# Performance work log

Hardware: AMD Instinct MI355X
Metric: run time of the kernel (lower is better)

The kernel has to match this reference:

```python
import jax, jax.numpy as jnp
import numpy as np

DOF = 7
DT = 0.1
MAX_VEL = 20.0
ACTION_RANGE = 50.0
BATCH = 16384


def skew(w):
    x, y, z = w[..., 0], w[..., 1], w[..., 2]
    o = jnp.zeros_like(x)
    return jnp.stack([jnp.stack([o, -z, y], -1),
                      jnp.stack([z, o, -x], -1),
                      jnp.stack([-y, x, o], -1)], -2)


def exp6(xi):
    # xi: (..., 6) twist [omega, v] (angular first). General se(3) exponential.
    w, v = xi[..., :3], xi[..., 3:]
    th = jnp.linalg.norm(w, axis=-1)                     # (...)
    small = th < 1e-10
    th_s = jnp.where(small, 1.0, th)
    W = skew(w / th_s[..., None])
    W2 = W @ W
    s, c = jnp.sin(th), jnp.cos(th)
    I3 = jnp.eye(3, dtype=xi.dtype)
    R = I3 + s[..., None, None] * W + (1.0 - c)[..., None, None] * W2
    Gm = th[..., None, None] * I3 + (1.0 - c)[..., None, None] * W + (th - s)[..., None, None] * W2
    p = jnp.einsum('...ij,...j->...i', Gm, v / th_s[..., None])
    R = jnp.where(small[..., None, None], I3, R)
    p = jnp.where(small[..., None], v, p)
    top = jnp.concatenate([R, p[..., None]], -1)
    bot = jnp.broadcast_to(jnp.array([0., 0., 0., 1.], xi.dtype), top.shape[:-2] + (1, 4))
    return jnp.concatenate([top, bot], -2)


def trans_inv(T):
    R = T[..., :3, :3]
    p = T[..., :3, 3]
    Rt = jnp.swapaxes(R, -1, -2)
    pi = -jnp.einsum('...ij,...j->...i', Rt, p)
    top = jnp.concatenate([Rt, pi[..., None]], -1)
    bot = jnp.broadcast_to(jnp.array([0., 0., 0., 1.], T.dtype), top.shape[:-2] + (1, 4))
    return jnp.concatenate([top, bot], -2)


def adjoint(T):
    R = T[..., :3, :3]
    p = T[..., :3, 3]
    pR = skew(p) @ R
    z = jnp.zeros_like(R)
    return jnp.concatenate([jnp.concatenate([R, z], -1),
                            jnp.concatenate([pR, R], -1)], -2)


def ad(V):
    w, v = V[..., :3], V[..., 3:]
    W, Vm = skew(w), skew(v)
    z = jnp.zeros_like(W)
    return jnp.concatenate([jnp.concatenate([W, z], -1),
                            jnp.concatenate([Vm, W], -1)], -2)


def inverse_dynamics(q, dq, ddq, gravity, ftip, Mlist, Glist, A):
    # Newton-Euler inverse dynamics (Modern Robotics), batched over B.
    B, n = q.shape
    dt = q.dtype
    V = jnp.zeros((B, 6), dt)
    Vd = jnp.concatenate([jnp.zeros((B, 3), dt), -jnp.broadcast_to(gravity, (B, 3))], -1)
    AdTs, Vs, Vds = [], [], []
    for i in range(n):  # forward recursion over joints (small fixed dof)
        Ti = exp6(-A[i] * q[:, i, None]) @ trans_inv(Mlist[i])   # (B,4,4)
        AdTi = adjoint(Ti)                                       # (B,6,6)
        V = jnp.einsum('bij,bj->bi', AdTi, V) + A[i] * dq[:, i, None]
        Vd = (jnp.einsum('bij,bj->bi', AdTi, Vd) + A[i] * ddq[:, i, None]
              + jnp.einsum('bij,j->bi', ad(V), A[i]) * dq[:, i, None])
        AdTs.append(AdTi)
        Vs.append(V)
        Vds.append(Vd)
    AdTs.append(jnp.broadcast_to(adjoint(trans_inv(Mlist[n])), (B, 6, 6)))
    F = jnp.broadcast_to(ftip, (B, 6))
    taus = [None] * n
    for i in range(n - 1, -1, -1):  # backward recursion
        GV = jnp.einsum('ij,bj->bi', Glist[i], Vs[i])
        F = (jnp.einsum('bji,bj->bi', AdTs[i + 1], F)
             + jnp.einsum('ij,bj->bi', Glist[i], Vds[i])
             - jnp.einsum('bji,bj->bi', ad(Vs[i]), GV))
        taus[i] = jnp.sum(F * A[i], -1)
    return jnp.stack(taus, -1)  # (B, n)


def forward_dynamics(q, dq, tau, gravity, ftip, Mlist, Glist, A):
    n = q.shape[1]
    z = jnp.zeros_like(q)
    g0 = jnp.zeros(3, q.dtype)
    f0 = jnp.zeros(6, q.dtype)
    # mass matrix columns via unit-ddq inverse dynamics
    cols = jax.vmap(lambda e: inverse_dynamics(q, z, jnp.broadcast_to(e, q.shape),
                                               g0, f0, Mlist, Glist, A))(jnp.eye(n, dtype=q.dtype))
    Mmat = jnp.transpose(cols, (1, 2, 0))                        # (B,n,n)
    # coriolis + gravity + end-effector bias in one pass (ddq=0)
    h = inverse_dynamics(q, dq, z, gravity, ftip, Mlist, Glist, A)
    return jnp.linalg.solve(Mmat, (tau - h)[..., None])[..., 0]


def _forward(state, torque, M_param, A, G_param, gravity, ftip):
    n = DOF
    # M property: keep top 3 rows, force bottom row to [0,0,0,1]
    bot = jnp.broadcast_to(jnp.array([0., 0., 0., 1.], M_param.dtype), (n + 1, 1, 4))
    Mlist = jnp.concatenate([M_param[:, :3], bot], axis=1)       # (n+1,4,4)
    # G property: diag(Ixx,Iyy,Izz,m,m,m)
    dvec = jnp.concatenate([G_param[:, :3], jnp.repeat(G_param[:, 3:4], 3, axis=1)], -1)
    Glist = dvec[:, :, None] * jnp.eye(6, dtype=G_param.dtype)   # (n,6,6)
    tau = torque * ACTION_RANGE

    def derivs(s, t):
        qpos, qvel, qf = s[..., :n], s[..., n:2 * n], s[..., 2 * n:3 * n]
        qacc = forward_dynamics(qpos, qvel, qf, gravity, ftip, Mlist, Glist, A)
        return jnp.concatenate([qvel, qacc, jnp.zeros_like(qf)], -1)

    s0 = jnp.concatenate([state, tau], -1)
    dt = DT
    k1 = derivs(s0, 0.0)
    k2 = derivs(s0 + 0.5 * dt * k1, 0.5 * dt)
    k3 = derivs(s0 + 0.5 * dt * k2, 0.5 * dt)
    k4 = derivs(s0 + dt * k3, dt)
    s1 = s0 + (dt / 6.0) * (k1 + 2.0 * k2 + 2.0 * k3 + k4)
    ns = s1[..., :2 * n]
    q = (ns[..., :n] + jnp.pi) % (2.0 * jnp.pi) - jnp.pi
    dq = jnp.clip(ns[..., n:], -MAX_VEL, MAX_VEL)
    # fk_in_space: chain link transforms, last frame is end-effector
    B = q.shape[0]
    T = jnp.broadcast_to(jnp.eye(4, dtype=q.dtype), (B, 4, 4))
    for i in range(n):
        T = T @ Mlist[i] @ exp6(A[i] * q[:, i, None])
    T = T @ Mlist[n]
    ee = T[:, :3, 3]
    return jnp.concatenate([q, dq], -1), ee


def setup_inputs() -> dict:
    key = jax.random.key(0)
    ks = jax.random.split(key, 6)
    state = jax.random.normal(ks[0], (BATCH, 2 * DOF), jnp.float32)
    torque = jax.random.normal(ks[1], (BATCH, DOF), jnp.float32)
    M_param = jnp.eye(4, dtype=jnp.float32)[None] + 0.05 * jax.random.normal(ks[2], (DOF + 1, 4, 4), jnp.float32)
    A = jax.random.uniform(ks[3], (DOF, 6), jnp.float32)
    G_param = jax.random.uniform(ks[4], (DOF, 4), jnp.float32, minval=0.1, maxval=1.0)
    gravity = jnp.array([0.0, -9.8, 0.0], jnp.float32)
    ftip = jnp.zeros(6, jnp.float32)
    return {"state": state, "torque": torque, "M_param": M_param, "A": A,
            "G_param": G_param, "gravity": gravity, "ftip": ftip}


def reference(state, torque, M_param, A, G_param, gravity, ftip):
    return _forward(state, torque, M_param, A, G_param, gravity, ftip)
```

## Files before the change

### kernel.cpp

```cpp
#include <hip/hip_runtime.h>
#include <math.h>

#define NB 16384

struct SConsts {
  float MrT[8][9];
  float mp[8][3];
  float A[7][6];
  float Gd[7][6];
  float X7p[3];
  float g[3];
  float ftip[6];
};

__device__ __forceinline__ void syncw() {
  __builtin_amdgcn_sched_barrier(0);
  __builtin_amdgcn_wave_barrier();
  __builtin_amdgcn_sched_barrier(0);
}

__device__ __forceinline__ float dot6(const float* a, const float* b) {
  return a[0]*b[0]+a[1]*b[1]+a[2]*b[2]+a[3]*b[3]+a[4]*b[4]+a[5]*b[5];
}

__device__ __forceinline__ void exp6_dev(float wx, float wy, float wz,
                                         float vx, float vy, float vz,
                                         float R[9], float p[3]) {
  float th2 = wx*wx + wy*wy + wz*wz;
  float th  = __builtin_amdgcn_sqrtf(th2);
  bool sm = th < 1e-10f;
  float ths = sm ? 1.0f : th;
  float inv = __builtin_amdgcn_rcpf(ths);
  float ux = wx*inv, uy = wy*inv, uz = wz*inv;
  float s = __sinf(th);
  float c = __cosf(th);
  float omc = 1.0f - c;
  float r00 = c + omc*ux*ux;
  float r01 = omc*ux*uy - s*uz;
  float r02 = omc*ux*uz + s*uy;
  float r10 = omc*uy*ux + s*uz;
  float r11 = c + omc*uy*uy;
  float r12 = omc*uy*uz - s*ux;
  float r20 = omc*uz*ux - s*uy;
  float r21 = omc*uz*uy + s*ux;
  float r22 = c + omc*uz*uz;
  float k1 = omc*inv, k2 = (th - s)*inv;
  float cx = uy*vz - uz*vy, cy = uz*vx - ux*vz, cz = ux*vy - uy*vx;
  float udv = ux*vx + uy*vy + uz*vz;
  float px = vx + k1*cx + k2*(ux*udv - vx);
  float py = vy + k1*cy + k2*(uy*udv - vy);
  float pz = vz + k1*cz + k2*(uz*udv - vz);
  R[0]=sm?1.f:r00; R[1]=sm?0.f:r01; R[2]=sm?0.f:r02;
  R[3]=sm?0.f:r10; R[4]=sm?1.f:r11; R[5]=sm?0.f:r12;
  R[6]=sm?0.f:r20; R[7]=sm?0.f:r21; R[8]=sm?1.f:r22;
  p[0]=sm?vx:px; p[1]=sm?vy:py; p[2]=sm?vz:pz;
}

__device__ __forceinline__ void Xapply(const float* R, const float* p,
                                       const float in[6], float out[6]) {
  float a = R[0]*in[0]+R[1]*in[1]+R[2]*in[2];
  float b = R[3]*in[0]+R[4]*in[1]+R[5]*in[2];
  float c = R[6]*in[0]+R[7]*in[1]+R[8]*in[2];
  float d = R[0]*in[3]+R[1]*in[4]+R[2]*in[5];
  float e = R[3]*in[3]+R[4]*in[4]+R[5]*in[5];
  float f = R[6]*in[3]+R[7]*in[4]+R[8]*in[5];
  out[0]=a; out[1]=b; out[2]=c;
  out[3] = p[1]*c - p[2]*b + d;
  out[4] = p[2]*a - p[0]*c + e;
  out[5] = p[0]*b - p[1]*a + f;
}

__device__ __forceinline__ void XTapply(const float* R, const float* p,
                                        const float in[6], float out[6]) {
  float fx=in[3], fy=in[4], fz=in[5];
  float tx = in[0] - (p[1]*fz - p[2]*fy);
  float ty = in[1] - (p[2]*fx - p[0]*fz);
  float tz = in[2] - (p[0]*fy - p[1]*fx);
  out[0] = R[0]*tx + R[3]*ty + R[6]*tz;
  out[1] = R[1]*tx + R[4]*ty + R[7]*tz;
  out[2] = R[2]*tx + R[5]*ty + R[8]*tz;
  out[3] = R[0]*fx + R[3]*fy + R[6]*fz;
  out[4] = R[1]*fx + R[4]*fy + R[7]*fz;
  out[5] = R[2]*fx + R[5]*fy + R[8]*fz;
}

extern "C" __global__ void __launch_bounds__(64, 2)
arm_kernel(const float* __restrict__ state, const float* __restrict__ torque,
           const float* __restrict__ Mp, const float* __restrict__ Ain,
           const float* __restrict__ Gp, const float* __restrict__ grav,
           const float* __restrict__ ftip_in, float* __restrict__ out)
{
  __shared__ SConsts C;
  __shared__ float XL[8][100];
  __shared__ float CL[8][68];
  const int t = threadIdx.x;

  {
    int i = t >> 3;
    #pragma unroll
    for (int kk = (t & 7); kk < 12; kk += 8) {
      if (kk < 9) {
        int r = kk / 3, c = kk - 3*(kk/3);
        C.MrT[i][c*3 + r] = Mp[i*16 + r*4 + c];
      } else {
        int r = kk - 9;
        C.mp[i][r] = Mp[i*16 + r*4 + 3];
      }
    }
    if (t < 42) {
      int i2 = t / 6, k = t - 6*(t/6);
      C.A[i2][k] = Ain[t];
      C.Gd[i2][k] = (k < 3) ? Gp[i2*4 + k] : Gp[i2*4 + 3];
    }
    if (t < 3) C.g[t] = grav[t];
    if (t < 6) C.ftip[t] = ftip_in[t];
  }
  syncw();
  if (t < 3)
    C.X7p[t] = -(C.MrT[7][t*3+0]*C.mp[7][0] + C.MrT[7][t*3+1]*C.mp[7][1] + C.MrT[7][t*3+2]*C.mp[7][2]);
  syncw();

  const int sub = t & 7;
  const int e   = t >> 3;
  const int b   = blockIdx.x * 8 + e;
  const int subc = (sub < 7) ? sub : 6;

  float dq0[7], tau[7], dqs[7];
  #pragma unroll
  for (int k = 0; k < 7; ++k) {
    dq0[k] = state[b*14 + 7 + k];
    tau[k] = torque[b*7 + k] * 50.0f;
    dqs[k] = dq0[k];
  }
  float q0s  = state[b*14 + subc];
  float dq0s = dq0[0];
  #pragma unroll
  for (int k = 1; k < 7; ++k) dq0s = (subc == k) ? dq0[k] : dq0s;

  float qss = q0s, dqss = dq0s;
  float accqs = 0.0f, accdqs = 0.0f;
  float a[7];
  const float gm = (sub == 7) ? 1.0f : 0.0f;

  #pragma unroll 1
  for (int stage = 0; stage < 4; ++stage) {
    syncw();
    if (sub < 7) {
      float Re[9], pe[3];
      exp6_dev(-C.A[sub][0]*qss, -C.A[sub][1]*qss, -C.A[sub][2]*qss,
               -C.A[sub][3]*qss, -C.A[sub][4]*qss, -C.A[sub][5]*qss, Re, pe);
      float Xr[12];
      #pragma unroll
      for (int r = 0; r < 3; ++r) {
        #pragma unroll
        for (int c = 0; c < 3; ++c)
          Xr[r*3+c] = Re[r*3+0]*C.MrT[sub][0+c] + Re[r*3+1]*C.MrT[sub][3+c] + Re[r*3+2]*C.MrT[sub][6+c];
      }
      #pragma unroll
      for (int r = 0; r < 3; ++r)
        Xr[9+r] = pe[r] - (Xr[r*3+0]*C.mp[sub][0] + Xr[r*3+1]*C.mp[sub][1] + Xr[r*3+2]*C.mp[sub][2]);
      float4* dst = (float4*)&XL[e][sub*12];
      dst[0] = make_float4(Xr[0],Xr[1],Xr[2],Xr[3]);
      dst[1] = make_float4(Xr[4],Xr[5],Xr[6],Xr[7]);
      dst[2] = make_float4(Xr[8],Xr[9],Xr[10],Xr[11]);
    }
    syncw();

    float X[7][12];
    #pragma unroll
    for (int i = 0; i < 7; ++i) {
      const float4* sx = (const float4*)&XL[e][i*12];
      float4 x0 = sx[0], x1 = sx[1], x2 = sx[2];
      X[i][0]=x0.x; X[i][1]=x0.y; X[i][2]=x0.z; X[i][3]=x0.w;
      X[i][4]=x1.x; X[i][5]=x1.y; X[i][6]=x1.z; X[i][7]=x1.w;
      X[i][8]=x2.x; X[i][9]=x2.y; X[i][10]=x2.z; X[i][11]=x2.w;
    }

    float V[6] = {0,0,0,0,0,0};
    float Vd[6];
    Vd[0]=0.0f; Vd[1]=0.0f; Vd[2]=0.0f;
    Vd[3] = -gm*C.g[0]; Vd[4] = -gm*C.g[1]; Vd[5] = -gm*C.g[2];
    float Fb[7][6];
    #pragma unroll
    for (int i = 0; i < 7; ++i) {
      float dqi  = (sub == 7) ? dqs[i] : 0.0f;
      float ddqi = (sub == i) ? 1.0f : 0.0f;
      float tv[6];
      Xapply(X[i], X[i]+9, V, tv);
      #pragma unroll
      for (int k = 0; k < 6; ++k) V[k] = tv[k] + C.A[i][k]*dqi;
      Xapply(X[i], X[i]+9, Vd, tv);
      float wx=V[0],wy=V[1],wz=V[2],vx=V[3],vy=V[4],vz=V[5];
      float ax=C.A[i][0],ay=C.A[i][1],az=C.A[i][2];
      float bx=C.A[i][3],by=C.A[i][4],bz=C.A[i][5];
      Vd[0] = tv[0] + ax*ddqi + (wy*az - wz*ay)*dqi;
      Vd[1] = tv[1] + ay*ddqi + (wz*ax - wx*az)*dqi;
      Vd[2] = tv[2] + az*ddqi + (wx*ay - wy*ax)*dqi;
      Vd[3] = tv[3] + bx*ddqi + (vy*az - vz*ay + wy*bz - wz*by)*dqi;
      Vd[4] = tv[4] + by*ddqi + (vz*ax - vx*az + wz*bx - wx*bz)*dqi;
      Vd[5] = tv[5] + bz*ddqi + (vx*ay - vy*ax + wx*by - wy*bx)*dqi;
      float g0=C.Gd[i][0], g1=C.Gd[i][1], g2=C.Gd[i][2], m=C.Gd[i][3];
      float Gt0=g0*wx, Gt1=g1*wy, Gt2=g2*wz;
      float Gb0=m*vx,  Gb1=m*vy,  Gb2=m*vz;
      Fb[i][0] = g0*Vd[0] + (wy*Gt2 - wz*Gt1) + (vy*Gb2 - vz*Gb1);
      Fb[i][1] = g1*Vd[1] + (wz*Gt0 - wx*Gt2) + (vz*Gb0 - vx*Gb2);
      Fb[i][2] = g2*Vd[2] + (wx*Gt1 - wy*Gt0) + (vx*Gb1 - vy*Gb0);
      Fb[i][3] = m*Vd[3] + (wy*Gb2 - wz*Gb1);
      Fb[i][4] = m*Vd[4] + (wz*Gb0 - wx*Gb2);
      Fb[i][5] = m*Vd[5] + (wx*Gb1 - wy*Gb0);
    }
    float col[7];
    float F[6];
    #pragma unroll
    for (int k = 0; k < 6; ++k) F[k] = gm*C.ftip[k];
    #pragma unroll
    for (int i = 6; i >= 0; --i) {
      float tv[6];
      if (i == 6) XTapply(C.MrT[7], C.X7p, F, tv);
      else        XTapply(X[i+1], X[i+1]+9, F, tv);
      #pragma unroll
      for (int k = 0; k < 6; ++k) F[k] = tv[k] + Fb[i][k];
      col[i] = dot6(F, C.A[i]);
    }

    syncw();
    #pragma unroll
    for (int k = 0; k < 7; ++k) CL[e][k*8 + sub] = col[k];
    syncw();
    float Mm[7][7], rhs[7];
    #pragma unroll
    for (int i = 0; i < 7; ++i) {
      const float4* rp = (const float4*)&CL[e][i*8];
      float4 r0 = rp[0], r1 = rp[1];
      Mm[i][0]=r0.x; Mm[i][1]=r0.y; Mm[i][2]=r0.z; Mm[i][3]=r0.w;
      Mm[i][4]=r1.x; Mm[i][5]=r1.y; Mm[i][6]=r1.z;
      rhs[i] = tau[i] - r1.w;
    }

    float invd[7];
    #pragma unroll
    for (int k = 0; k < 7; ++k) {
      invd[k] = __builtin_amdgcn_rcpf(Mm[k][k]);
      #pragma unroll
      for (int i2 = k+1; i2 < 7; ++i2) {
        float f = Mm[i2][k] * invd[k];
        #pragma unroll
        for (int c2 = k+1; c2 < 7; ++c2) Mm[i2][c2] -= f * Mm[k][c2];
        rhs[i2] -= f * rhs[k];
      }
    }
    #pragma unroll
    for (int i2 = 6; i2 >= 0; --i2) {
      float s = rhs[i2];
      #pragma unroll
      for (int c2 = i2+1; c2 < 7; ++c2) s -= Mm[i2][c2] * a[c2];
      a[i2] = s * invd[i2];
    }

    float a_own = a[0];
    #pragma unroll
    for (int k = 1; k < 7; ++k) a_own = (subc == k) ? a[k] : a_own;
    float w = (stage == 1 || stage == 2) ? 2.0f : 1.0f;
    accqs  += w*dqss;
    accdqs += w*a_own;
    if (stage < 3) {
      float cc = (stage == 2) ? 0.1f : 0.05f;
      qss  = q0s + cc*dqss;
      dqss = dq0s + cc*a_own;
      #pragma unroll
      for (int k = 0; k < 7; ++k) dqs[k] = dq0[k] + cc*a[k];
    }
  }

  const float c6 = (float)(0.1/6.0);
  const float PI_F = 3.14159265358979323846f;
  const float TWO_PI_F = 6.28318530717958647692f;
  const float INV_TWO_PI_F = 0.15915494309189535f;
  float q1 = q0s  + c6*accqs;
  float d1 = dq0s + c6*accdqs;
  float x = q1 + PI_F;
  float n = floorf(x * INV_TWO_PI_F);
  float y = fmaf(n, -TWO_PI_F, x);
  y = (y < 0.0f) ? y + TWO_PI_F : y;
  y = (y >= TWO_PI_F) ? y - TWO_PI_F : y;
  float qw_own  = y - PI_F;
  float dqw_own = fminf(fmaxf(d1, -20.0f), 20.0f);
  if (sub < 7) {
    out[b*14 + sub]     = qw_own;
    out[b*14 + 7 + sub] = dqw_own;
  }

  syncw();
  if (sub < 7) {
    float Re[9], pe[3];
    exp6_dev(C.A[sub][0]*qw_own, C.A[sub][1]*qw_own, C.A[sub][2]*qw_own,
             C.A[sub][3]*qw_own, C.A[sub][4]*qw_own, C.A[sub][5]*qw_own, Re, pe);
    float L[12];
    #pragma unroll
    for (int r = 0; r < 3; ++r) {
      #pragma unroll
      for (int c = 0; c < 3; ++c)
        L[r*3+c] = C.MrT[sub][0*3+r]*Re[0*3+c] + C.MrT[sub][1*3+r]*Re[1*3+c] + C.MrT[sub][2*3+r]*Re[2*3+c];
      L[9+r] = C.MrT[sub][0*3+r]*pe[0] + C.MrT[sub][1*3+r]*pe[1] + C.MrT[sub][2*3+r]*pe[2] + C.mp[sub][r];
    }
    float4* dst = (float4*)&XL[e][sub*12];
    dst[0] = make_float4(L[0],L[1],L[2],L[3]);
    dst[1] = make_float4(L[4],L[5],L[6],L[7]);
    dst[2] = make_float4(L[8],L[9],L[10],L[11]);
  }
  syncw();
  float X2[7][12];
  #pragma unroll
  for (int i = 0; i < 7; ++i) {
    const float4* sx = (const float4*)&XL[e][i*12];
    float4 x0 = sx[0], x1 = sx[1], x2 = sx[2];
    X2[i][0]=x0.x; X2[i][1]=x0.y; X2[i][2]=x0.z; X2[i][3]=x0.w;
    X2[i][4]=x1.x; X2[i][5]=x1.y; X2[i][6]=x1.z; X2[i][7]=x1.w;
    X2[i][8]=x2.x; X2[i][9]=x2.y; X2[i][10]=x2.z; X2[i][11]=x2.w;
  }
  float v0 = C.mp[7][0], v1 = C.mp[7][1], v2 = C.mp[7][2];
  #pragma unroll
  for (int i = 6; i >= 0; --i) {
    float n0 = X2[i][0]*v0 + X2[i][1]*v1 + X2[i][2]*v2 + X2[i][9];
    float n1 = X2[i][3]*v0 + X2[i][4]*v1 + X2[i][5]*v2 + X2[i][10];
    float n2 = X2[i][6]*v0 + X2[i][7]*v1 + X2[i][8]*v2 + X2[i][11];
    v0 = n0; v1 = n1; v2 = n2;
  }
  {
    float ev = v0;
    ev = (sub == 1) ? v1 : ev;
    ev = (sub == 2) ? v2 : ev;
    if (sub < 3) out[NB*14 + b*3 + sub] = ev;
  }
}

extern "C" void kernel_launch(void* const* d_in, const int* in_sizes, int n_in,
                              void* d_out, int out_size, void* d_ws, size_t ws_size,
                              hipStream_t stream) {
  const float* state  = (const float*)d_in[0];
  const float* torque = (const float*)d_in[1];
  const float* Mp     = (const float*)d_in[2];
  const float* Ain    = (const float*)d_in[3];
  const float* Gp     = (const float*)d_in[4];
  const float* grav   = (const float*)d_in[5];
  const float* ftip   = (const float*)d_in[6];
  float* out = (float*)d_out;
  hipLaunchKernelGGL(arm_kernel, dim3(NB/8), dim3(64), 0, stream,
                     state, torque, Mp, Ain, Gp, grav, ftip, out);
}
```

Before: 26.53 us.

## Replace backward force recursion with shared-memory Jacobian-based mass matrix columns

The backward Newton-Euler force pass is replaced. Each sub-lane stores its per-link unit-acceleration twist in shared memory, and mass-matrix columns are then formed as dot products of the link wrenches with the stored twists, plus a tip-force term. The 7x12 transform arrays are no longer kept in registers; rows are re-read from LDS where needed, which lowers register pressure. The cost is a large shared-memory buffer of about 12.5 KB per block and many LDS reads, which may limit occupancy or bank bandwidth.

```diff
diff --git a/kernel.cpp b/kernel.cpp
--- a/kernel.cpp
+++ b/kernel.cpp
@@ -70,20 +70,6 @@
   out[5] = p[0]*b - p[1]*a + f;
 }
 
-__device__ __forceinline__ void XTapply(const float* R, const float* p,
-                                        const float in[6], float out[6]) {
-  float fx=in[3], fy=in[4], fz=in[5];
-  float tx = in[0] - (p[1]*fz - p[2]*fy);
-  float ty = in[1] - (p[2]*fx - p[0]*fz);
-  float tz = in[2] - (p[0]*fy - p[1]*fx);
-  out[0] = R[0]*tx + R[3]*ty + R[6]*tz;
-  out[1] = R[1]*tx + R[4]*ty + R[7]*tz;
-  out[2] = R[2]*tx + R[5]*ty + R[8]*tz;
-  out[3] = R[0]*fx + R[3]*fy + R[6]*fz;
-  out[4] = R[1]*fx + R[4]*fy + R[7]*fz;
-  out[5] = R[2]*fx + R[5]*fy + R[8]*fz;
-}
-
 extern "C" __global__ void __launch_bounds__(64, 2)
 arm_kernel(const float* __restrict__ state, const float* __restrict__ torque,
            const float* __restrict__ Mp, const float* __restrict__ Ain,
@@ -93,6 +79,8 @@
   __shared__ SConsts C;
   __shared__ float XL[8][100];
   __shared__ float CL[8][68];
+  __shared__ float JL[8*7*7*8];
+  __shared__ float TD[8][8];
   const int t = threadIdx.x;
 
   {
@@ -166,16 +154,6 @@
     }
     syncw();
 
-    float X[7][12];
-    #pragma unroll
-    for (int i = 0; i < 7; ++i) {
-      const float4* sx = (const float4*)&XL[e][i*12];
-      float4 x0 = sx[0], x1 = sx[1], x2 = sx[2];
-      X[i][0]=x0.x; X[i][1]=x0.y; X[i][2]=x0.z; X[i][3]=x0.w;
-      X[i][4]=x1.x; X[i][5]=x1.y; X[i][6]=x1.z; X[i][7]=x1.w;
-      X[i][8]=x2.x; X[i][9]=x2.y; X[i][10]=x2.z; X[i][11]=x2.w;
-    }
-
     float V[6] = {0,0,0,0,0,0};
     float Vd[6];
     Vd[0]=0.0f; Vd[1]=0.0f; Vd[2]=0.0f;
@@ -183,13 +161,16 @@
     float Fb[7][6];
     #pragma unroll
     for (int i = 0; i < 7; ++i) {
+      const float4* sx = (const float4*)&XL[e][i*12];
+      float4 x0 = sx[0], x1 = sx[1], x2 = sx[2];
+      float Xr[12] = {x0.x,x0.y,x0.z,x0.w, x1.x,x1.y,x1.z,x1.w, x2.x,x2.y,x2.z,x2.w};
       float dqi  = (sub == 7) ? dqs[i] : 0.0f;
       float ddqi = (sub == i) ? 1.0f : 0.0f;
       float tv[6];
-      Xapply(X[i], X[i]+9, V, tv);
+      Xapply(Xr, Xr+9, V, tv);
       #pragma unroll
       for (int k = 0; k < 6; ++k) V[k] = tv[k] + C.A[i][k]*dqi;
-      Xapply(X[i], X[i]+9, Vd, tv);
+      Xapply(Xr, Xr+9, Vd, tv);
       float wx=V[0],wy=V[1],wz=V[2],vx=V[3],vy=V[4],vz=V[5];
       float ax=C.A[i][0],ay=C.A[i][1],az=C.A[i][2];
       float bx=C.A[i][3],by=C.A[i][4],bz=C.A[i][5];
@@ -199,6 +180,11 @@
       Vd[3] = tv[3] + bx*ddqi + (vy*az - vz*ay + wy*bz - wz*by)*dqi;
       Vd[4] = tv[4] + by*ddqi + (vz*ax - vx*az + wz*bx - wx*bz)*dqi;
       Vd[5] = tv[5] + bz*ddqi + (vx*ay - vy*ax + wx*by - wy*bx)*dqi;
+      if (sub < 7) {
+        float* jp = &JL[((e*7 + i)*7 + sub)*8];
+        *(float4*)jp = make_float4(Vd[0], Vd[1], Vd[2], Vd[3]);
+        *(float2*)(jp + 4) = make_float2(Vd[4], Vd[5]);
+      }
       float g0=C.Gd[i][0], g1=C.Gd[i][1], g2=C.Gd[i][2], m=C.Gd[i][3];
       float Gt0=g0*wx, Gt1=g1*wy, Gt2=g2*wz;
       float Gb0=m*vx,  Gb1=m*vy,  Gb2=m*vz;
@@ -209,21 +195,29 @@
       Fb[i][4] = m*Vd[4] + (wz*Gb0 - wx*Gb2);
       Fb[i][5] = m*Vd[5] + (wx*Gb1 - wy*Gb0);
     }
-    float col[7];
-    float F[6];
-    #pragma unroll
-    for (int k = 0; k < 6; ++k) F[k] = gm*C.ftip[k];
-    #pragma unroll
-    for (int i = 6; i >= 0; --i) {
-      float tv[6];
-      if (i == 6) XTapply(C.MrT[7], C.X7p, F, tv);
-      else        XTapply(X[i+1], X[i+1]+9, F, tv);
-      #pragma unroll
-      for (int k = 0; k < 6; ++k) F[k] = tv[k] + Fb[i][k];
-      col[i] = dot6(F, C.A[i]);
-    }
-
+    {
+      float jt[6];
+      Xapply(C.MrT[7], C.X7p, Vd, jt);
+      float td = dot6(jt, C.ftip);
+      if (sub < 7) TD[e][sub] = td;
+    }
     syncw();
+
+    float col[7] = {0,0,0,0,0,0,0};
+    #pragma unroll
+    for (int k = 0; k < 7; ++k) {
+      #pragma unroll
+      for (int i = 0; i <= k; ++i) {
+        const float* jp = &JL[((e*7 + k)*7 + i)*8];
+        float4 j0 = *(const float4*)jp;
+        float2 j1 = *(const float2*)(jp + 4);
+        col[i] += Fb[k][0]*j0.x + Fb[k][1]*j0.y + Fb[k][2]*j0.z
+                + Fb[k][3]*j0.w + Fb[k][4]*j1.x + Fb[k][5]*j1.y;
+      }
+    }
+    #pragma unroll
+    for (int i = 0; i < 7; ++i) col[i] += gm * TD[e][i];
+
     #pragma unroll
     for (int k = 0; k < 7; ++k) CL[e][k*8 + sub] = col[k];
     syncw();
@@ -309,21 +303,14 @@
     dst[2] = make_float4(L[8],L[9],L[10],L[11]);
   }
   syncw();
-  float X2[7][12];
-  #pragma unroll
-  for (int i = 0; i < 7; ++i) {
-    const float4* sx = (const float4*)&XL[e][i*12];
-    float4 x0 = sx[0], x1 = sx[1], x2 = sx[2];
-    X2[i][0]=x0.x; X2[i][1]=x0.y; X2[i][2]=x0.z; X2[i][3]=x0.w;
-    X2[i][4]=x1.x; X2[i][5]=x1.y; X2[i][6]=x1.z; X2[i][7]=x1.w;
-    X2[i][8]=x2.x; X2[i][9]=x2.y; X2[i][10]=x2.z; X2[i][11]=x2.w;
-  }
   float v0 = C.mp[7][0], v1 = C.mp[7][1], v2 = C.mp[7][2];
   #pragma unroll
   for (int i = 6; i >= 0; --i) {
-    float n0 = X2[i][0]*v0 + X2[i][1]*v1 + X2[i][2]*v2 + X2[i][9];
-    float n1 = X2[i][3]*v0 + X2[i][4]*v1 + X2[i][5]*v2 + X2[i][10];
-    float n2 = X2[i][6]*v0 + X2[i][7]*v1 + X2[i][8]*v2 + X2[i][11];
+    const float4* sx = (const float4*)&XL[e][i*12];
+    float4 x0 = sx[0], x1 = sx[1], x2 = sx[2];
+    float n0 = x0.x*v0 + x0.y*v1 + x0.z*v2 + x2.y;
+    float n1 = x0.w*v0 + x1.x*v1 + x1.y*v2 + x2.z;
+    float n2 = x1.z*v0 + x1.w*v1 + x2.x*v2 + x2.w;
     v0 = n0; v1 = n1; v2 = n2;
   }
   {
```

New measurement: 34.64 us. 30.6% more time.

## Process two batch elements per 8-lane group to raise per-thread ILP

Applied to the files above, without the earlier changes.

Each 8-lane group now handles two batch elements, interleaving their exp6 builds, RNEA passes, 7x7 solves and FK chains. The grid is halved to 1024 blocks and shared buffers are doubled. RNEA now reads the transforms from LDS per step instead of caching them all in registers, and the launch bound drops to one wave minimum. The aim is more independent work per thread to hide latency and to amortise the per-block constant load, at the cost of higher register pressure and fewer waves per CU.

```diff
diff --git a/kernel.cpp b/kernel.cpp
--- a/kernel.cpp
+++ b/kernel.cpp
@@ -84,15 +84,117 @@
   out[5] = R[2]*fx + R[5]*fy + R[8]*fz;
 }
 
-extern "C" __global__ void __launch_bounds__(64, 2)
+__device__ __forceinline__ void build_X(const SConsts& C, int sub, float q,
+                                        float* XLe) {
+  float Re[9], pe[3];
+  exp6_dev(-C.A[sub][0]*q, -C.A[sub][1]*q, -C.A[sub][2]*q,
+           -C.A[sub][3]*q, -C.A[sub][4]*q, -C.A[sub][5]*q, Re, pe);
+  float Xr[12];
+  #pragma unroll
+  for (int r = 0; r < 3; ++r) {
+    #pragma unroll
+    for (int c = 0; c < 3; ++c)
+      Xr[r*3+c] = Re[r*3+0]*C.MrT[sub][0+c] + Re[r*3+1]*C.MrT[sub][3+c] + Re[r*3+2]*C.MrT[sub][6+c];
+  }
+  #pragma unroll
+  for (int r = 0; r < 3; ++r)
+    Xr[9+r] = pe[r] - (Xr[r*3+0]*C.mp[sub][0] + Xr[r*3+1]*C.mp[sub][1] + Xr[r*3+2]*C.mp[sub][2]);
+  float4* dst = (float4*)XLe;
+  dst[0] = make_float4(Xr[0],Xr[1],Xr[2],Xr[3]);
+  dst[1] = make_float4(Xr[4],Xr[5],Xr[6],Xr[7]);
+  dst[2] = make_float4(Xr[8],Xr[9],Xr[10],Xr[11]);
+}
+
+__device__ __forceinline__ void rnea_pass(const SConsts& C, const float* XLe,
+                                          const float dqs[7], int sub, float gm,
+                                          float col[7]) {
+  float V[6] = {0,0,0,0,0,0};
+  float Vd[6];
+  Vd[0]=0.0f; Vd[1]=0.0f; Vd[2]=0.0f;
+  Vd[3] = -gm*C.g[0]; Vd[4] = -gm*C.g[1]; Vd[5] = -gm*C.g[2];
+  float Fb[7][6];
+  #pragma unroll
+  for (int i = 0; i < 7; ++i) {
+    const float4* sx = (const float4*)&XLe[i*12];
+    float4 x0 = sx[0], x1 = sx[1], x2 = sx[2];
+    float Xr[12] = {x0.x,x0.y,x0.z,x0.w, x1.x,x1.y,x1.z,x1.w, x2.x,x2.y,x2.z,x2.w};
+    float dqi  = (sub == 7) ? dqs[i] : 0.0f;
+    float ddqi = (sub == i) ? 1.0f : 0.0f;
+    float tv[6];
+    Xapply(Xr, Xr+9, V, tv);
+    #pragma unroll
+    for (int k = 0; k < 6; ++k) V[k] = tv[k] + C.A[i][k]*dqi;
+    Xapply(Xr, Xr+9, Vd, tv);
+    float wx=V[0],wy=V[1],wz=V[2],vx=V[3],vy=V[4],vz=V[5];
+    float ax=C.A[i][0],ay=C.A[i][1],az=C.A[i][2];
+    float bx=C.A[i][3],by=C.A[i][4],bz=C.A[i][5];
+    Vd[0] = tv[0] + ax*ddqi + (wy*az - wz*ay)*dqi;
+    Vd[1] = tv[1] + ay*ddqi + (wz*ax - wx*az)*dqi;
+    Vd[2] = tv[2] + az*ddqi + (wx*ay - wy*ax)*dqi;
+    Vd[3] = tv[3] + bx*ddqi + (vy*az - vz*ay + wy*bz - wz*by)*dqi;
+    Vd[4] = tv[4] + by*ddqi + (vz*ax - vx*az + wz*bx - wx*bz)*dqi;
+    Vd[5] = tv[5] + bz*ddqi + (vx*ay - vy*ax + wx*by - wy*bx)*dqi;
+    float g0=C.Gd[i][0], g1=C.Gd[i][1], g2=C.Gd[i][2], m=C.Gd[i][3];
+    float Gt0=g0*wx, Gt1=g1*wy, Gt2=g2*wz;
+    float Gb0=m*vx,  Gb1=m*vy,  Gb2=m*vz;
+    Fb[i][0] = g0*Vd[0] + (wy*Gt2 - wz*Gt1) + (vy*Gb2 - vz*Gb1);
+    Fb[i][1] = g1*Vd[1] + (wz*Gt0 - wx*Gt2) + (vz*Gb0 - vx*Gb2);
+    Fb[i][2] = g2*Vd[2] + (wx*Gt1 - wy*Gt0) + (vx*Gb1 - vy*Gb0);
+    Fb[i][3] = m*Vd[3] + (wy*Gb2 - wz*Gb1);
+    Fb[i][4] = m*Vd[4] + (wz*Gb0 - wx*Gb2);
+    Fb[i][5] = m*Vd[5] + (wx*Gb1 - wy*Gb0);
+  }
+  float F[6];
+  #pragma unroll
+  for (int k = 0; k < 6; ++k) F[k] = gm*C.ftip[k];
+  #pragma unroll
+  for (int i = 6; i >= 0; --i) {
+    float tv[6];
+    if (i == 6) {
+      XTapply(C.MrT[7], C.X7p, F, tv);
+    } else {
+      const float4* sx = (const float4*)&XLe[(i+1)*12];
+      float4 x0 = sx[0], x1 = sx[1], x2 = sx[2];
+      float Xr[12] = {x0.x,x0.y,x0.z,x0.w, x1.x,x1.y,x1.z,x1.w, x2.x,x2.y,x2.z,x2.w};
+      XTapply(Xr, Xr+9, F, tv);
+    }
+    #pragma unroll
+    for (int k = 0; k < 6; ++k) F[k] = tv[k] + Fb[i][k];
+    col[i] = dot6(F, C.A[i]);
+  }
+}
+
+__device__ __forceinline__ void solve7(float Mm[7][7], float rhs[7], float a[7]) {
+  float invd[7];
+  #pragma unroll
+  for (int k = 0; k < 7; ++k) {
+    invd[k] = __builtin_amdgcn_rcpf(Mm[k][k]);
+    #pragma unroll
+    for (int i2 = k+1; i2 < 7; ++i2) {
+      float f = Mm[i2][k] * invd[k];
+      #pragma unroll
+      for (int c2 = k+1; c2 < 7; ++c2) Mm[i2][c2] -= f * Mm[k][c2];
+      rhs[i2] -= f * rhs[k];
+    }
+  }
+  #pragma unroll
+  for (int i2 = 6; i2 >= 0; --i2) {
+    float s = rhs[i2];
+    #pragma unroll
+    for (int c2 = i2+1; c2 < 7; ++c2) s -= Mm[i2][c2] * a[c2];
+    a[i2] = s * invd[i2];
+  }
+}
+
+extern "C" __global__ void __launch_bounds__(64, 1)
 arm_kernel(const float* __restrict__ state, const float* __restrict__ torque,
            const float* __restrict__ Mp, const float* __restrict__ Ain,
            const float* __restrict__ Gp, const float* __restrict__ grav,
            const float* __restrict__ ftip_in, float* __restrict__ out)
 {
   __shared__ SConsts C;
-  __shared__ float XL[8][100];
-  __shared__ float CL[8][68];
+  __shared__ float XL[16][100];
+  __shared__ float CL[16][68];
   const int t = threadIdx.x;
 
   {
@@ -118,219 +220,181 @@
   syncw();
   if (t < 3)
     C.X7p[t] = -(C.MrT[7][t*3+0]*C.mp[7][0] + C.MrT[7][t*3+1]*C.mp[7][1] + C.MrT[7][t*3+2]*C.mp[7][2]);
-  syncw();
 
   const int sub = t & 7;
-  const int e   = t >> 3;
-  const int b   = blockIdx.x * 8 + e;
+  const int g   = t >> 3;
+  const int eA  = g*2, eB = g*2 + 1;
+  const int bA  = blockIdx.x * 16 + eA;
+  const int bB  = bA + 1;
   const int subc = (sub < 7) ? sub : 6;
 
-  float dq0[7], tau[7], dqs[7];
+  float dq0A[7], tauA[7], dqsA[7], dq0B[7], tauB[7], dqsB[7];
   #pragma unroll
   for (int k = 0; k < 7; ++k) {
-    dq0[k] = state[b*14 + 7 + k];
-    tau[k] = torque[b*7 + k] * 50.0f;
-    dqs[k] = dq0[k];
-  }
-  float q0s  = state[b*14 + subc];
-  float dq0s = dq0[0];
-  #pragma unroll
-  for (int k = 1; k < 7; ++k) dq0s = (subc == k) ? dq0[k] : dq0s;
-
-  float qss = q0s, dqss = dq0s;
-  float accqs = 0.0f, accdqs = 0.0f;
-  float a[7];
+    dq0A[k] = state[bA*14 + 7 + k];
+    tauA[k] = torque[bA*7 + k] * 50.0f;
+    dqsA[k] = dq0A[k];
+    dq0B[k] = state[bB*14 + 7 + k];
+    tauB[k] = torque[bB*7 + k] * 50.0f;
+    dqsB[k] = dq0B[k];
+  }
+  float q0sA = state[bA*14 + subc];
+  float q0sB = state[bB*14 + subc];
+  float dq0sA = dq0A[0], dq0sB = dq0B[0];
+  #pragma unroll
+  for (int k = 1; k < 7; ++k) {
+    dq0sA = (subc == k) ? dq0A[k] : dq0sA;
+    dq0sB = (subc == k) ? dq0B[k] : dq0sB;
+  }
+
+  float qssA = q0sA, dqssA = dq0sA, accqA = 0.0f, accdqA = 0.0f;
+  float qssB = q0sB, dqssB = dq0sB, accqB = 0.0f, accdqB = 0.0f;
+  float aA[7], aB[7];
   const float gm = (sub == 7) ? 1.0f : 0.0f;
 
   #pragma unroll 1
   for (int stage = 0; stage < 4; ++stage) {
     syncw();
     if (sub < 7) {
+      build_X(C, sub, qssA, &XL[eA][sub*12]);
+      build_X(C, sub, qssB, &XL[eB][sub*12]);
+    }
+    syncw();
+
+    float colA[7], colB[7];
+    rnea_pass(C, &XL[eA][0], dqsA, sub, gm, colA);
+    rnea_pass(C, &XL[eB][0], dqsB, sub, gm, colB);
+
+    syncw();
+    #pragma unroll
+    for (int k = 0; k < 7; ++k) {
+      CL[eA][k*8 + sub] = colA[k];
+      CL[eB][k*8 + sub] = colB[k];
+    }
+    syncw();
+    float MmA[7][7], rhsA[7], MmB[7][7], rhsB[7];
+    #pragma unroll
+    for (int i = 0; i < 7; ++i) {
+      const float4* rpA = (const float4*)&CL[eA][i*8];
+      float4 a0 = rpA[0], a1 = rpA[1];
+      MmA[i][0]=a0.x; MmA[i][1]=a0.y; MmA[i][2]=a0.z; MmA[i][3]=a0.w;
+      MmA[i][4]=a1.x; MmA[i][5]=a1.y; MmA[i][6]=a1.z;
+      rhsA[i] = tauA[i] - a1.w;
+      const float4* rpB = (const float4*)&CL[eB][i*8];
+      float4 b0 = rpB[0], b1 = rpB[1];
+      MmB[i][0]=b0.x; MmB[i][1]=b0.y; MmB[i][2]=b0.z; MmB[i][3]=b0.w;
+      MmB[i][4]=b1.x; MmB[i][5]=b1.y; MmB[i][6]=b1.z;
+      rhsB[i] = tauB[i] - b1.w;
+    }
+
+    solve7(MmA, rhsA, aA);
+    solve7(MmB, rhsB, aB);
+
+    float aoA = aA[0], aoB = aB[0];
+    #pragma unroll
+    for (int k = 1; k < 7; ++k) {
+      aoA = (subc == k) ? aA[k] : aoA;
+      aoB = (subc == k) ? aB[k] : aoB;
+    }
+    float w = (stage == 1 || stage == 2) ? 2.0f : 1.0f;
+    accqA += w*dqssA;  accdqA += w*aoA;
+    accqB += w*dqssB;  accdqB += w*aoB;
+    if (stage < 3) {
+      float cc = (stage == 2) ? 0.1f : 0.05f;
+      qssA  = q0sA + cc*dqssA;
+      dqssA = dq0sA + cc*aoA;
+      qssB  = q0sB + cc*dqssB;
+      dqssB = dq0sB + cc*aoB;
+      #pragma unroll
+      for (int k = 0; k < 7; ++k) {
+        dqsA[k] = dq0A[k] + cc*aA[k];
+        dqsB[k] = dq0B[k] + cc*aB[k];
+      }
+    }
+  }
+
+  const float c6 = (float)(0.1/6.0);
+  const float PI_F = 3.14159265358979323846f;
+  const float TWO_PI_F = 6.28318530717958647692f;
+  const float INV_TWO_PI_F = 0.15915494309189535f;
+  float qwA, dqwA, qwB, dqwB;
+  {
+    float q1 = q0sA + c6*accqA;
+    float d1 = dq0sA + c6*accdqA;
+    float x = q1 + PI_F;
+    float n = floorf(x * INV_TWO_PI_F);
+    float y = fmaf(n, -TWO_PI_F, x);
+    y = (y < 0.0f) ? y + TWO_PI_F : y;
+    y = (y >= TWO_PI_F) ? y - TWO_PI_F : y;
+    qwA = y - PI_F;
+    dqwA = fminf(fmaxf(d1, -20.0f), 20.0f);
+  }
+  {
+    float q1 = q0sB + c6*accqB;
+    float d1 = dq0sB + c6*accdqB;
+    float x = q1 + PI_F;
+    float n = floorf(x * INV_TWO_PI_F);
+    float y = fmaf(n, -TWO_PI_F, x);
+    y = (y < 0.0f) ? y + TWO_PI_F : y;
+    y = (y >= TWO_PI_F) ? y - TWO_PI_F : y;
+    qwB = y - PI_F;
+    dqwB = fminf(fmaxf(d1, -20.0f), 20.0f);
+  }
+  if (sub < 7) {
+    out[bA*14 + sub]     = qwA;
+    out[bA*14 + 7 + sub] = dqwA;
+    out[bB*14 + sub]     = qwB;
+    out[bB*14 + 7 + sub] = dqwB;
+  }
+
+  syncw();
+  if (sub < 7) {
+    #pragma unroll
+    for (int el = 0; el < 2; ++el) {
+      float qw_own = (el == 0) ? qwA : qwB;
       float Re[9], pe[3];
-      exp6_dev(-C.A[sub][0]*qss, -C.A[sub][1]*qss, -C.A[sub][2]*qss,
-               -C.A[sub][3]*qss, -C.A[sub][4]*qss, -C.A[sub][5]*qss, Re, pe);
-      float Xr[12];
+      exp6_dev(C.A[sub][0]*qw_own, C.A[sub][1]*qw_own, C.A[sub][2]*qw_own,
+               C.A[sub][3]*qw_own, C.A[sub][4]*qw_own, C.A[sub][5]*qw_own, Re, pe);
+      float L[12];
       #pragma unroll
       for (int r = 0; r < 3; ++r) {
         #pragma unroll
         for (int c = 0; c < 3; ++c)
-          Xr[r*3+c] = Re[r*3+0]*C.MrT[sub][0+c] + Re[r*3+1]*C.MrT[sub][3+c] + Re[r*3+2]*C.MrT[sub][6+c];
+          L[r*3+c] = C.MrT[sub][0*3+r]*Re[0*3+c] + C.MrT[sub][1*3+r]*Re[1*3+c] + C.MrT[sub][2*3+r]*Re[2*3+c];
+        L[9+r] = C.MrT[sub][0*3+r]*pe[0] + C.MrT[sub][1*3+r]*pe[1] + C.MrT[sub][2*3+r]*pe[2] + C.mp[sub][r];
       }
-      #pragma unroll
-      for (int r = 0; r < 3; ++r)
-        Xr[9+r] = pe[r] - (Xr[r*3+0]*C.mp[sub][0] + Xr[r*3+1]*C.mp[sub][1] + Xr[r*3+2]*C.mp[sub][2]);
-      float4* dst = (float4*)&XL[e][sub*12];
-      dst[0] = make_float4(Xr[0],Xr[1],Xr[2],Xr[3]);
-      dst[1] = make_float4(Xr[4],Xr[5],Xr[6],Xr[7]);
-      dst[2] = make_float4(Xr[8],Xr[9],Xr[10],Xr[11]);
-    }
-    syncw();
-
-    float X[7][12];
-    #pragma unroll
-    for (int i = 0; i < 7; ++i) {
-      const float4* sx = (const float4*)&XL[e][i*12];
-      float4 x0 = sx[0], x1 = sx[1], x2 = sx[2];
-      X[i][0]=x0.x; X[i][1]=x0.y; X[i][2]=x0.z; X[i][3]=x0.w;
-      X[i][4]=x1.x; X[i][5]=x1.y; X[i][6]=x1.z; X[i][7]=x1.w;
-      X[i][8]=x2.x; X[i][9]=x2.y; X[i][10]=x2.z; X[i][11]=x2.w;
-    }
-
-    float V[6] = {0,0,0,0,0,0};
-    float Vd[6];
-    Vd[0]=0.0f; Vd[1]=0.0f; Vd[2]=0.0f;
-    Vd[3] = -gm*C.g[0]; Vd[4] = -gm*C.g[1]; Vd[5] = -gm*C.g[2];
-    float Fb[7][6];
-    #pragma unroll
-    for (int i = 0; i < 7; ++i) {
-      float dqi  = (sub == 7) ? dqs[i] : 0.0f;
-      float ddqi = (sub == i) ? 1.0f : 0.0f;
-      float tv[6];
-      Xapply(X[i], X[i]+9, V, tv);
-      #pragma unroll
-      for (int k = 0; k < 6; ++k) V[k] = tv[k] + C.A[i][k]*dqi;
-      Xapply(X[i], X[i]+9, Vd, tv);
-      float wx=V[0],wy=V[1],wz=V[2],vx=V[3],vy=V[4],vz=V[5];
-      float ax=C.A[i][0],ay=C.A[i][1],az=C.A[i][2];
-      float bx=C.A[i][3],by=C.A[i][4],bz=C.A[i][5];
-      Vd[0] = tv[0] + ax*ddqi + (wy*az - wz*ay)*dqi;
-      Vd[1] = tv[1] + ay*ddqi + (wz*ax - wx*az)*dqi;
-      Vd[2] = tv[2] + az*ddqi + (wx*ay - wy*ax)*dqi;
-      Vd[3] = tv[3] + bx*ddqi + (vy*az - vz*ay + wy*bz - wz*by)*dqi;
-      Vd[4] = tv[4] + by*ddqi + (vz*ax - vx*az + wz*bx - wx*bz)*dqi;
-      Vd[5] = tv[5] + bz*ddqi + (vx*ay - vy*ax + wx*by - wy*bx)*dqi;
-      float g0=C.Gd[i][0], g1=C.Gd[i][1], g2=C.Gd[i][2], m=C.Gd[i][3];
-      float Gt0=g0*wx, Gt1=g1*wy, Gt2=g2*wz;
-      float Gb0=m*vx,  Gb1=m*vy,  Gb2=m*vz;
-      Fb[i][0] = g0*Vd[0] + (wy*Gt2 - wz*Gt1) + (vy*Gb2 - vz*Gb1);
-      Fb[i][1] = g1*Vd[1] + (wz*Gt0 - wx*Gt2) + (vz*Gb0 - vx*Gb2);
-      Fb[i][2] = g2*Vd[2] + (wx*Gt1 - wy*Gt0) + (vx*Gb1 - vy*Gb0);
-      Fb[i][3] = m*Vd[3] + (wy*Gb2 - wz*Gb1);
-      Fb[i][4] = m*Vd[4] + (wz*Gb0 - wx*Gb2);
-      Fb[i][5] = m*Vd[5] + (wx*Gb1 - wy*Gb0);
-    }
-    float col[7];
-    float F[6];
-    #pragma unroll
-    for (int k = 0; k < 6; ++k) F[k] = gm*C.ftip[k];
-    #pragma unroll
-    for (int i = 6; i >= 0; --i) {
-      float tv[6];
-      if (i == 6) XTapply(C.MrT[7], C.X7p, F, tv);
-      else        XTapply(X[i+1], X[i+1]+9, F, tv);
-      #pragma unroll
-      for (int k = 0; k < 6; ++k) F[k] = tv[k] + Fb[i][k];
-      col[i] = dot6(F, C.A[i]);
-    }
-
-    syncw();
-    #pragma unroll
-    for (int k = 0; k < 7; ++k) CL[e][k*8 + sub] = col[k];
-    syncw();
-    float Mm[7][7], rhs[7];
-    #pragma unroll
-    for (int i = 0; i < 7; ++i) {
-      const float4* rp = (const float4*)&CL[e][i*8];
-      float4 r0 = rp[0], r1 = rp[1];
-      Mm[i][0]=r0.x; Mm[i][1]=r0.y; Mm[i][2]=r0.z; Mm[i][3]=r0.w;
-      Mm[i][4]=r1.x; Mm[i][5]=r1.y; Mm[i][6]=r1.z;
-      rhs[i] = tau[i] - r1.w;
-    }
-
-    float invd[7];
-    #pragma unroll
-    for (int k = 0; k < 7; ++k) {
-      invd[k] = __builtin_amdgcn_rcpf(Mm[k][k]);
-      #pragma unroll
-      for (int i2 = k+1; i2 < 7; ++i2) {
-        float f = Mm[i2][k] * invd[k];
-        #pragma unroll
-        for (int c2 = k+1; c2 < 7; ++c2) Mm[i2][c2] -= f * Mm[k][c2];
-        rhs[i2] -= f * rhs[k];
-      }
-    }
-    #pragma unroll
-    for (int i2 = 6; i2 >= 0; --i2) {
-      float s = rhs[i2];
-      #pragma unroll
-      for (int c2 = i2+1; c2 < 7; ++c2) s -= Mm[i2][c2] * a[c2];
-      a[i2] = s * invd[i2];
-    }
-
-    float a_own = a[0];
-    #pragma unroll
-    for (int k = 1; k < 7; ++k) a_own = (subc == k) ? a[k] : a_own;
-    float w = (stage == 1 || stage == 2) ? 2.0f : 1.0f;
-    accqs  += w*dqss;
-    accdqs += w*a_own;
-    if (stage < 3) {
-      float cc = (stage == 2) ? 0.1f : 0.05f;
-      qss  = q0s + cc*dqss;
-      dqss = dq0s + cc*a_own;
-      #pragma unroll
-      for (int k = 0; k < 7; ++k) dqs[k] = dq0[k] + cc*a[k];
-    }
-  }
-
-  const float c6 = (float)(0.1/6.0);
-  const float PI_F = 3.14159265358979323846f;
-  const float TWO_PI_F = 6.28318530717958647692f;
-  const float INV_TWO_PI_F = 0.15915494309189535f;
-  float q1 = q0s  + c6*accqs;
-  float d1 = dq0s + c6*accdqs;
-  float x = q1 + PI_F;
-  float n = floorf(x * INV_TWO_PI_F);
-  float y = fmaf(n, -TWO_PI_F, x);
-  y = (y < 0.0f) ? y + TWO_PI_F : y;
-  y = (y >= TWO_PI_F) ? y - TWO_PI_F : y;
-  float qw_own  = y - PI_F;
-  float dqw_own = fminf(fmaxf(d1, -20.0f), 20.0f);
-  if (sub < 7) {
-    out[b*14 + sub]     = qw_own;
-    out[b*14 + 7 + sub] = dqw_own;
-  }
-
+      float4* dst = (float4*)&XL[(el == 0) ? eA : eB][sub*12];
+      dst[0] = make_float4(L[0],L[1],L[2],L[3]);
+      dst[1] = make_float4(L[4],L[5],L[6],L[7]);
+      dst[2] = make_float4(L[8],L[9],L[10],L[11]);
+    }
+  }
   syncw();
-  if (sub < 7) {
-    float Re[9], pe[3];
-    exp6_dev(C.A[sub][0]*qw_own, C.A[sub][1]*qw_own, C.A[sub][2]*qw_own,
-             C.A[sub][3]*qw_own, C.A[sub][4]*qw_own, C.A[sub][5]*qw_own, Re, pe);
-    float L[12];
-    #pragma unroll
-    for (int r = 0; r < 3; ++r) {
-      #pragma unroll
-      for (int c = 0; c < 3; ++c)
-        L[r*3+c] = C.MrT[sub][0*3+r]*Re[0*3+c] + C.MrT[sub][1*3+r]*Re[1*3+c] + C.MrT[sub][2*3+r]*Re[2*3+c];
-      L[9+r] = C.MrT[sub][0*3+r]*pe[0] + C.MrT[sub][1*3+r]*pe[1] + C.MrT[sub][2*3+r]*pe[2] + C.mp[sub][r];
-    }
-    float4* dst = (float4*)&XL[e][sub*12];
-    dst[0] = make_float4(L[0],L[1],L[2],L[3]);
-    dst[1] = make_float4(L[4],L[5],L[6],L[7]);
-    dst[2] = make_float4(L[8],L[9],L[10],L[11]);
-  }
-  syncw();
-  float X2[7][12];
-  #pragma unroll
-  for (int i = 0; i < 7; ++i) {
-    const float4* sx = (const float4*)&XL[e][i*12];
-    float4 x0 = sx[0], x1 = sx[1], x2 = sx[2];
-    X2[i][0]=x0.x; X2[i][1]=x0.y; X2[i][2]=x0.z; X2[i][3]=x0.w;
-    X2[i][4]=x1.x; X2[i][5]=x1.y; X2[i][6]=x1.z; X2[i][7]=x1.w;
-    X2[i][8]=x2.x; X2[i][9]=x2.y; X2[i][10]=x2.z; X2[i][11]=x2.w;
-  }
-  float v0 = C.mp[7][0], v1 = C.mp[7][1], v2 = C.mp[7][2];
+  float vA0 = C.mp[7][0], vA1 = C.mp[7][1], vA2 = C.mp[7][2];
+  float vB0 = vA0, vB1 = vA1, vB2 = vA2;
   #pragma unroll
   for (int i = 6; i >= 0; --i) {
-    float n0 = X2[i][0]*v0 + X2[i][1]*v1 + X2[i][2]*v2 + X2[i][9];
-    float n1 = X2[i][3]*v0 + X2[i][4]*v1 + X2[i][5]*v2 + X2[i][10];
-    float n2 = X2[i][6]*v0 + X2[i][7]*v1 + X2[i][8]*v2 + X2[i][11];
-    v0 = n0; v1 = n1; v2 = n2;
+    const float4* sA = (const float4*)&XL[eA][i*12];
+    float4 a0 = sA[0], a1 = sA[1], a2 = sA[2];
+    float nA0 = a0.x*vA0 + a0.y*vA1 + a0.z*vA2 + a2.y;
+    float nA1 = a0.w*vA0 + a1.x*vA1 + a1.y*vA2 + a2.z;
+    float nA2 = a1.z*vA0 + a1.w*vA1 + a2.x*vA2 + a2.w;
+    vA0 = nA0; vA1 = nA1; vA2 = nA2;
+    const float4* sB = (const float4*)&XL[eB][i*12];
+    float4 b0 = sB[0], b1 = sB[1], b2 = sB[2];
+    float nB0 = b0.x*vB0 + b0.y*vB1 + b0.z*vB2 + b2.y;
+    float nB1 = b0.w*vB0 + b1.x*vB1 + b1.y*vB2 + b2.z;
+    float nB2 = b1.z*vB0 + b1.w*vB1 + b2.x*vB2 + b2.w;
+    vB0 = nB0; vB1 = nB1; vB2 = nB2;
   }
   {
-    float ev = v0;
-    ev = (sub == 1) ? v1 : ev;
-    ev = (sub == 2) ? v2 : ev;
-    if (sub < 3) out[NB*14 + b*3 + sub] = ev;
+    float evA = vA0, evB = vB0;
+    evA = (sub == 1) ? vA1 : evA;  evB = (sub == 1) ? vB1 : evB;
+    evA = (sub == 2) ? vA2 : evA;  evB = (sub == 2) ? vB2 : evB;
+    if (sub < 3) {
+      out[NB*14 + bA*3 + sub] = evA;
+      out[NB*14 + bB*3 + sub] = evB;
+    }
   }
 }
 
@@ -345,6 +409,6 @@
   const float* grav   = (const float*)d_in[5];
   const float* ftip   = (const float*)d_in[6];
   float* out = (float*)d_out;
-  hipLaunchKernelGGL(arm_kernel, dim3(NB/8), dim3(64), 0, stream,
+  hipLaunchKernelGGL(arm_kernel, dim3(NB/16), dim3(64), 0, stream,
                      state, torque, Mp, Ain, Gp, grav, ftip, out);
 }
```

After: 33.77 us. 27.3% more time.

## Distribute 7x7 mass-matrix solve across lanes with shuffles, stagger block starts

Applied to the files above, without the earlier changes.

Replaces the redundant per-lane Gaussian elimination, where every lane loaded the whole mass matrix from LDS and solved it, with a row-distributed elimination in which each lane owns one row. Pivot rows and back-substitution values are exchanged with width-8 shuffles, and the CL shared buffer is removed. Each lane now loads only its own torque, and the final FK loop reads XL per step instead of preloading all 84 values. It also adds s_sleep staggering by block index, meant to spread out contention at kernel start. The change cuts register pressure and redundant FLOPs, but puts a chain of shuffles on the serial critical path.

```diff
diff --git a/kernel.cpp b/kernel.cpp
--- a/kernel.cpp
+++ b/kernel.cpp
@@ -92,8 +92,14 @@
 {
   __shared__ SConsts C;
   __shared__ float XL[8][100];
-  __shared__ float CL[8][68];
   const int t = threadIdx.x;
+
+  switch (blockIdx.x & 3) {
+    case 1: __builtin_amdgcn_s_sleep(2); break;
+    case 2: __builtin_amdgcn_s_sleep(4); break;
+    case 3: __builtin_amdgcn_s_sleep(6); break;
+    default: break;
+  }
 
   {
     int i = t >> 3;
@@ -125,13 +131,13 @@
   const int b   = blockIdx.x * 8 + e;
   const int subc = (sub < 7) ? sub : 6;
 
-  float dq0[7], tau[7], dqs[7];
+  float dq0[7], dqs[7];
   #pragma unroll
   for (int k = 0; k < 7; ++k) {
     dq0[k] = state[b*14 + 7 + k];
-    tau[k] = torque[b*7 + k] * 50.0f;
     dqs[k] = dq0[k];
   }
+  float tau_own = torque[b*7 + subc] * 50.0f;
   float q0s  = state[b*14 + subc];
   float dq0s = dq0[0];
   #pragma unroll
@@ -223,38 +229,43 @@
       col[i] = dot6(F, C.A[i]);
     }
 
-    syncw();
-    #pragma unroll
-    for (int k = 0; k < 7; ++k) CL[e][k*8 + sub] = col[k];
-    syncw();
-    float Mm[7][7], rhs[7];
-    #pragma unroll
-    for (int i = 0; i < 7; ++i) {
-      const float4* rp = (const float4*)&CL[e][i*8];
-      float4 r0 = rp[0], r1 = rp[1];
-      Mm[i][0]=r0.x; Mm[i][1]=r0.y; Mm[i][2]=r0.z; Mm[i][3]=r0.w;
-      Mm[i][4]=r1.x; Mm[i][5]=r1.y; Mm[i][6]=r1.z;
-      rhs[i] = tau[i] - r1.w;
-    }
-
-    float invd[7];
+    float rhs_own;
+    {
+      float h_own = __shfl(col[0], 7, 8);
+      #pragma unroll
+      for (int i = 1; i < 7; ++i) {
+        float hi = __shfl(col[i], 7, 8);
+        h_own = (subc == i) ? hi : h_own;
+      }
+      rhs_own = tau_own - h_own;
+    }
+
+    float row[7];
+    #pragma unroll
+    for (int c = 0; c < 7; ++c) row[c] = col[c];
+    float invd_own = 0.0f;
     #pragma unroll
     for (int k = 0; k < 7; ++k) {
-      invd[k] = __builtin_amdgcn_rcpf(Mm[k][k]);
-      #pragma unroll
-      for (int i2 = k+1; i2 < 7; ++i2) {
-        float f = Mm[i2][k] * invd[k];
-        #pragma unroll
-        for (int c2 = k+1; c2 < 7; ++c2) Mm[i2][c2] -= f * Mm[k][c2];
-        rhs[i2] -= f * rhs[k];
+      float pk    = __shfl(row[k], k, 8);
+      float prhs  = __shfl(rhs_own, k, 8);
+      float invpk = __builtin_amdgcn_rcpf(pk);
+      invd_own = (subc == k) ? invpk : invd_own;
+      float f = row[k] * invpk;
+      f = (sub > k) ? f : 0.0f;
+      #pragma unroll
+      for (int c = k+1; c < 7; ++c) {
+        float pc = __shfl(row[c], k, 8);
+        row[c] -= f * pc;
       }
-    }
-    #pragma unroll
-    for (int i2 = 6; i2 >= 0; --i2) {
-      float s = rhs[i2];
-      #pragma unroll
-      for (int c2 = i2+1; c2 < 7; ++c2) s -= Mm[i2][c2] * a[c2];
-      a[i2] = s * invd[i2];
+      rhs_own -= f * prhs;
+    }
+    #pragma unroll
+    for (int i = 6; i >= 0; --i) {
+      float s = rhs_own;
+      #pragma unroll
+      for (int c = i+1; c < 7; ++c) s -= row[c] * a[c];
+      float val = s * invd_own;
+      a[i] = __shfl(val, i, 8);
     }
 
     float a_own = a[0];
@@ -309,21 +320,14 @@
     dst[2] = make_float4(L[8],L[9],L[10],L[11]);
   }
   syncw();
-  float X2[7][12];
-  #pragma unroll
-  for (int i = 0; i < 7; ++i) {
-    const float4* sx = (const float4*)&XL[e][i*12];
-    float4 x0 = sx[0], x1 = sx[1], x2 = sx[2];
-    X2[i][0]=x0.x; X2[i][1]=x0.y; X2[i][2]=x0.z; X2[i][3]=x0.w;
-    X2[i][4]=x1.x; X2[i][5]=x1.y; X2[i][6]=x1.z; X2[i][7]=x1.w;
-    X2[i][8]=x2.x; X2[i][9]=x2.y; X2[i][10]=x2.z; X2[i][11]=x2.w;
-  }
   float v0 = C.mp[7][0], v1 = C.mp[7][1], v2 = C.mp[7][2];
   #pragma unroll
   for (int i = 6; i >= 0; --i) {
-    float n0 = X2[i][0]*v0 + X2[i][1]*v1 + X2[i][2]*v2 + X2[i][9];
-    float n1 = X2[i][3]*v0 + X2[i][4]*v1 + X2[i][5]*v2 + X2[i][10];
-    float n2 = X2[i][6]*v0 + X2[i][7]*v1 + X2[i][8]*v2 + X2[i][11];
+    const float4* sx = (const float4*)&XL[e][i*12];
+    float4 x0 = sx[0], x1 = sx[1], x2 = sx[2];
+    float n0 = x0.x*v0 + x0.y*v1 + x0.z*v2 + x2.y;
+    float n1 = x0.w*v0 + x1.x*v1 + x1.y*v2 + x2.z;
+    float n2 = x1.z*v0 + x1.w*v1 + x2.x*v2 + x2.w;
     v0 = n0; v1 = n1; v2 = n2;
   }
   {
```

Result: slower. 27.58 us (+4.0%).
